# Performance work log

Hardware: AMD Instinct MI355X
Metric: run time of the kernel (lower is better)

Reference implementation:

```python
import jax, jax.numpy as jnp
import numpy as np

NEG_SLOPE = 0.2
EPS = 1e-16


def setup_inputs() -> dict:
    key = jax.random.key(0)
    k1, k2, k3, k4 = jax.random.split(key, 4)
    N, H, F, E = 50000, 4, 32, 800000
    nodes_features = jax.random.normal(k1, (N, H, F), dtype=jnp.float32)
    edge_index = jax.random.randint(k2, (2, E), 0, N, dtype=jnp.int64)
    scoring_fn_source = jax.random.normal(k3, (1, H, F), dtype=jnp.float32)
    scoring_fn_target = jax.random.normal(k4, (1, H, F), dtype=jnp.float32)
    return {
        "nodes_features": nodes_features,
        "scoring_fn_source": scoring_fn_source,
        "scoring_fn_target": scoring_fn_target,
        "edge_index": edge_index,
    }


def reference(nodes_features, scoring_fn_source, scoring_fn_target, edge_index):
    # nodes_features: [N, H, F]; edge_index: [2, E] with row 0 = target, row 1 = source
    num_of_nodes = nodes_features.shape[0]
    trg = edge_index[0]
    src = edge_index[1]

    # Per-node attention logits per head: [N, H]
    scores_source = (nodes_features * scoring_fn_source).sum(axis=-1)
    scores_target = (nodes_features * scoring_fn_target).sum(axis=-1)

    # Lift N -> E via gather: [E, H]
    scores_lifted = scores_source[src] + scores_target[trg]
    src_nodes_features_lifted = nodes_features[src]  # [E, H, F]

    scores_per_edge = jax.nn.leaky_relu(scores_lifted, NEG_SLOPE)
    # Global max subtraction for numerical stability (matches original code)
    scores_per_edge = scores_per_edge - scores_per_edge.max()
    exp_scores = jnp.exp(scores_per_edge)

    # Segment softmax denominator via scatter-add, then gather back per edge
    neighborhood_sums = jax.ops.segment_sum(exp_scores, trg, num_segments=num_of_nodes)
    denom = neighborhood_sums[trg]  # [E, H]

    attentions_per_edge = (exp_scores / (denom + EPS))[..., None]  # [E, H, 1]
    return attentions_per_edge, src_nodes_features_lifted
```

## Files before the change

### kernel.cpp

```cpp
#include <hip/hip_runtime.h>

#define NEG_SLOPE 0.2f
#define EPSV 1e-16f

typedef float f32x4 __attribute__((ext_vector_type(4)));

__device__ __forceinline__ unsigned fenc(float f) {
    unsigned b = __float_as_uint(f);
    return b ^ ((b & 0x80000000u) ? 0xFFFFFFFFu : 0x80000000u);
}
__device__ __forceinline__ float fdec(unsigned u) {
    unsigned b = (u & 0x80000000u) ? (u ^ 0x80000000u) : ~u;
    return __uint_as_float(b);
}
#define FENC_NEG_INF 0x007FFFFFu

__global__ void detect_idx_kernel(const unsigned* __restrict__ ei32,
                                  int* __restrict__ flag) {
    __shared__ int anynz;
    if (threadIdx.x == 0) anynz = 0;
    __syncthreads();
    unsigned v = ei32[2 * threadIdx.x + 1];
    if (v != 0u) anynz = 1;
    __syncthreads();
    if (threadIdx.x == 0) *flag = (anynz ? 0 : 1);
}

__device__ __forceinline__ int load_idx(const void* ei, int is64, size_t k) {
    if (is64) return (int)__builtin_nontemporal_load(&((const long long*)ei)[k]);
    return __builtin_nontemporal_load(&((const int*)ei)[k]);
}

__global__ void node_scores_kernel(const float* __restrict__ nf,
                                   const float* __restrict__ sfs,
                                   const float* __restrict__ sft,
                                   float* __restrict__ ss,
                                   float* __restrict__ st,
                                   float* __restrict__ nsum,
                                   unsigned* __restrict__ gmax,
                                   int NH, int nzero) {
    int i = blockIdx.x * blockDim.x + threadIdx.x;
    if (i >= NH) return;
    if (i == 0) *gmax = FENC_NEG_INF;
    for (int k = i; k < nzero; k += NH) nsum[k] = 0.f;
    int h = i & 3;
    const float4* __restrict__ row = (const float4*)(nf + (size_t)i * 32);
    const float4* __restrict__ as  = (const float4*)(sfs + h * 32);
    const float4* __restrict__ at  = (const float4*)(sft + h * 32);
    float accs = 0.f, acct = 0.f;
#pragma unroll
    for (int q = 0; q < 8; ++q) {
        float4 v = row[q];
        float4 a = as[q];
        float4 b = at[q];
        accs += v.x * a.x + v.y * a.y + v.z * a.z + v.w * a.w;
        acct += v.x * b.x + v.y * b.y + v.z * b.z + v.w * b.w;
    }
    ss[i] = accs;
    st[i] = acct;
}

__global__ void combined_kernel(const void* __restrict__ ei,
                                const int* __restrict__ flag,
                                const f32x4* __restrict__ nf4,
                                const float* __restrict__ ss,
                                const float* __restrict__ st,
                                float* __restrict__ pbuf,
                                float* __restrict__ nsum,
                                unsigned* __restrict__ gmax,
                                f32x4* __restrict__ feat_out,
                                int E, int NS) {
    __shared__ float red[256];
    int is64 = *flag;
    int vbid = blockIdx.x >> 1;
    int vstride = (gridDim.x >> 1) * blockDim.x;

    if ((blockIdx.x & 1) == 0) {
        int n = E * 32;
        for (int t = vbid * blockDim.x + threadIdx.x; t < n; t += vstride) {
            int e = t >> 5, q = t & 31;
            int src = load_idx(ei, is64, (size_t)E + e);
            f32x4 v = nf4[(size_t)src * 32 + q];
            __builtin_nontemporal_store(v, &feat_out[(size_t)e * 32 + q]);
        }
    } else {
        int n4 = E * 4;
        float lmax = -__builtin_inff();
        for (int i = vbid * blockDim.x + threadIdx.x; i < n4; i += vstride) {
            int e = i >> 2, h = i & 3;
            int trg = load_idx(ei, is64, e);
            int src = load_idx(ei, is64, (size_t)E + e);
            float s = ss[src * 4 + h] + st[trg * 4 + h];
            float lr = s > 0.f ? s : NEG_SLOPE * s;
            lmax = fmaxf(lmax, lr);
            float p = __expf(lr);
            __builtin_nontemporal_store(p, &pbuf[i]);
            atomicAdd(&nsum[(size_t)trg * NS + h], p);
        }
        red[threadIdx.x] = lmax;
        __syncthreads();
        for (int off = 128; off > 0; off >>= 1) {
            if (threadIdx.x < off)
                red[threadIdx.x] = fmaxf(red[threadIdx.x], red[threadIdx.x + off]);
            __syncthreads();
        }
        if (threadIdx.x == 0) atomicMax(gmax, fenc(red[0]));
    }
}

__global__ void att_lean_kernel(const void* __restrict__ ei,
                                const int* __restrict__ flag,
                                const float* __restrict__ pbuf,
                                const float* __restrict__ nsum,
                                const unsigned* __restrict__ gmax,
                                float* __restrict__ out,
                                int E, int NS) {
    int is64 = *flag;
    float de = EPSV * __expf(fdec(*gmax));
    int stride = gridDim.x * blockDim.x;
    for (int e = blockIdx.x * blockDim.x + threadIdx.x; e < E; e += stride) {
        int trg = load_idx(ei, is64, e);
        f32x4 p = __builtin_nontemporal_load((const f32x4*)(pbuf + (size_t)e * 4));
        f32x4 d = *(const f32x4*)(nsum + (size_t)trg * NS);
        f32x4 a = p / (d + de);
        __builtin_nontemporal_store(a, (f32x4*)(out + (size_t)e * 4));
    }
}

__device__ __forceinline__ float edge_lr_rc(const void* ei, int is64,
                                            const float* ss, const float* st,
                                            int E, int e, int h, int* trg_out) {
    int trg = load_idx(ei, is64, e);
    int src = load_idx(ei, is64, (size_t)E + e);
    if (trg_out) *trg_out = trg;
    float s = ss[src * 4 + h] + st[trg * 4 + h];
    return s > 0.f ? s : NEG_SLOPE * s;
}

__global__ void edge_exp_sum_fb_kernel(const void* __restrict__ ei,
                                       const int* __restrict__ flag,
                                       const float* __restrict__ ss,
                                       const float* __restrict__ st,
                                       float* __restrict__ nsum,
                                       unsigned* __restrict__ gmax, int E) {
    __shared__ float red[256];
    int is64 = *flag;
    int n4 = E * 4;
    int stride = gridDim.x * blockDim.x;
    float lmax = -__builtin_inff();
    for (int i = blockIdx.x * blockDim.x + threadIdx.x; i < n4; i += stride) {
        int trg;
        float lr = edge_lr_rc(ei, is64, ss, st, E, i >> 2, i & 3, &trg);
        lmax = fmaxf(lmax, lr);
        atomicAdd(&nsum[trg * 4 + (i & 3)], __expf(lr));
    }
    red[threadIdx.x] = lmax;
    __syncthreads();
    for (int off = 128; off > 0; off >>= 1) {
        if (threadIdx.x < off)
            red[threadIdx.x] = fmaxf(red[threadIdx.x], red[threadIdx.x + off]);
        __syncthreads();
    }
    if (threadIdx.x == 0) atomicMax(gmax, fenc(red[0]));
}

__global__ void att_fb_kernel(const void* __restrict__ ei,
                              const int* __restrict__ flag,
                              const float* __restrict__ ss,
                              const float* __restrict__ st,
                              const unsigned* __restrict__ gmax,
                              const float* __restrict__ nsum,
                              float* __restrict__ out, int E) {
    int i = blockIdx.x * blockDim.x + threadIdx.x;
    if (i >= E * 4) return;
    int is64 = *flag;
    float de = EPSV * __expf(fdec(*gmax));
    int trg;
    float lr = edge_lr_rc(ei, is64, ss, st, E, i >> 2, i & 3, &trg);
    float a = __expf(lr) / (nsum[trg * 4 + (i & 3)] + de);
    __builtin_nontemporal_store(a, &out[i]);
}

__global__ void gather_feat_fb_kernel(const void* __restrict__ ei,
                                      const int* __restrict__ flag,
                                      const f32x4* __restrict__ nf4,
                                      f32x4* __restrict__ out4, int E) {
    int is64 = *flag;
    int n = E * 32;
    int stride = gridDim.x * blockDim.x;
    for (int t = blockIdx.x * blockDim.x + threadIdx.x; t < n; t += stride) {
        int e = t >> 5, q = t & 31;
        int src = load_idx(ei, is64, (size_t)E + e);
        f32x4 v = nf4[(size_t)src * 32 + q];
        __builtin_nontemporal_store(v, &out4[(size_t)e * 32 + q]);
    }
}

extern "C" void kernel_launch(void* const* d_in, const int* in_sizes, int n_in,
                              void* d_out, int out_size, void* d_ws, size_t ws_size,
                              hipStream_t stream) {
    const float* nf  = (const float*)d_in[0];
    const float* sfs = (const float*)d_in[1];
    const float* sft = (const float*)d_in[2];
    const void*  ei  = d_in[3];

    const int NH = in_sizes[0] / 32;
    const int N  = NH / 4;
    const int E  = in_sizes[3] / 2;

    float* out = (float*)d_out;
    float* ws  = (float*)d_ws;

    const int B = 256;

    float*    ss   = ws;
    float*    st   = ws + NH;
    int*      flag = (int*)(ws + 2 * (size_t)NH);
    unsigned* gmax = (unsigned*)(flag + 1);
    float*    pbuf = ws + 2 * (size_t)NH + 4;
    float*    nsum = pbuf + (size_t)E * 4;

    int NS = 0;
    for (int cand = 16; cand >= 4; cand >>= 2) {
        size_t need = ((size_t)2 * NH + 4 + (size_t)E * 4 + (size_t)N * cand) * 4;
        if (ws_size >= need) { NS = cand; break; }
    }

    detect_idx_kernel<<<1, 256, 0, stream>>>((const unsigned*)ei, flag);

    if (NS > 0) {
        node_scores_kernel<<<(NH + B - 1) / B, B, 0, stream>>>(
            nf, sfs, sft, ss, st, nsum, gmax, NH, N * NS);
        combined_kernel<<<8192, B, 0, stream>>>(ei, flag, (const f32x4*)nf,
                                                ss, st, pbuf, nsum, gmax,
                                                (f32x4*)(out + (size_t)E * 4),
                                                E, NS);
        att_lean_kernel<<<2048, B, 0, stream>>>(ei, flag, pbuf, nsum, gmax,
                                                out, E, NS);
    } else {
        float* nsum_fb = (float*)(gmax + 1);
        node_scores_kernel<<<(NH + B - 1) / B, B, 0, stream>>>(
            nf, sfs, sft, ss, st, nsum_fb, gmax, NH, NH);
        edge_exp_sum_fb_kernel<<<2048, B, 0, stream>>>(ei, flag, ss, st,
                                                       nsum_fb, gmax, E);
        att_fb_kernel<<<(E * 4 + B - 1) / B, B, 0, stream>>>(ei, flag, ss, st,
                                                             gmax, nsum_fb, out, E);
        gather_feat_fb_kernel<<<4096, B, 0, stream>>>(
            ei, flag, (const f32x4*)nf, (f32x4*)(out + (size_t)E * 4), E);
    }
}
```

Baseline: 256.0 us.

## Accumulate softmax denominators with packed bf16 atomics and split feature gather

Replaces the fp32 per-head atomicAdd into padded neighborhood sums with packed two-wide bf16 atomic adds (global_atomic_fadd_v2bf16, with a CAS fallback), so each edge issues two atomics instead of four and the sum array shrinks to 8 bytes per node. The feature gather no longer shares a kernel with the score pass and runs as its own launch after the attention pass. The padded-stride layout meant to spread atomic contention is dropped. bf16 accumulation of sums over about 16 edges per node loses precision, which may exceed the tolerance, and the separate gather gives up the overlap the combined kernel provided.

```diff
diff --git a/kernel.cpp b/kernel.cpp
--- a/kernel.cpp
+++ b/kernel.cpp
@@ -1,9 +1,13 @@
 #include <hip/hip_runtime.h>
+#include <hip/hip_bf16.h>
 
 #define NEG_SLOPE 0.2f
 #define EPSV 1e-16f
 
 typedef float f32x4 __attribute__((ext_vector_type(4)));
+typedef float f32x2 __attribute__((ext_vector_type(2)));
+typedef short s16x2 __attribute__((ext_vector_type(2)));
+typedef unsigned u32x2 __attribute__((ext_vector_type(2)));
 
 __device__ __forceinline__ unsigned fenc(float f) {
     unsigned b = __float_as_uint(f);
@@ -14,6 +18,31 @@
     return __uint_as_float(b);
 }
 #define FENC_NEG_INF 0x007FFFFFu
+
+__device__ __forceinline__ unsigned f32_to_bf16_rne(float f) {
+    unsigned u = __float_as_uint(f);
+    unsigned lsb = (u >> 16) & 1u;
+    return (u + 0x7FFFu + lsb) >> 16;
+}
+
+__device__ __forceinline__ void pk_atomic_add_bf16(unsigned* addr, float a, float b) {
+#if __has_builtin(__builtin_amdgcn_global_atomic_fadd_v2bf16)
+    s16x2 v;
+    v.x = (short)f32_to_bf16_rne(a);
+    v.y = (short)f32_to_bf16_rne(b);
+    typedef __attribute__((address_space(1))) s16x2 gs16x2;
+    __builtin_amdgcn_global_atomic_fadd_v2bf16((gs16x2*)(void*)addr, v);
+#else
+    unsigned old = *addr, assumed;
+    do {
+        assumed = old;
+        float lo = __uint_as_float((assumed & 0xFFFFu) << 16) + a;
+        float hi = __uint_as_float(assumed & 0xFFFF0000u) + b;
+        unsigned nv = (f32_to_bf16_rne(hi) << 16) | (f32_to_bf16_rne(lo) & 0xFFFFu);
+        old = atomicCAS(addr, assumed, nv);
+    } while (old != assumed);
+#endif
+}
 
 __global__ void detect_idx_kernel(const unsigned* __restrict__ ei32,
                                   int* __restrict__ flag) {
@@ -36,13 +65,13 @@
                                    const float* __restrict__ sft,
                                    float* __restrict__ ss,
                                    float* __restrict__ st,
-                                   float* __restrict__ nsum,
+                                   unsigned* __restrict__ nsum_zero,
                                    unsigned* __restrict__ gmax,
                                    int NH, int nzero) {
     int i = blockIdx.x * blockDim.x + threadIdx.x;
     if (i >= NH) return;
     if (i == 0) *gmax = FENC_NEG_INF;
-    for (int k = i; k < nzero; k += NH) nsum[k] = 0.f;
+    for (int k = i; k < nzero; k += NH) nsum_zero[k] = 0u;
     int h = i & 3;
     const float4* __restrict__ row = (const float4*)(nf + (size_t)i * 32);
     const float4* __restrict__ as  = (const float4*)(sfs + h * 32);
@@ -60,70 +89,80 @@
     st[i] = acct;
 }
 
-__global__ void combined_kernel(const void* __restrict__ ei,
-                                const int* __restrict__ flag,
-                                const f32x4* __restrict__ nf4,
-                                const float* __restrict__ ss,
-                                const float* __restrict__ st,
-                                float* __restrict__ pbuf,
-                                float* __restrict__ nsum,
-                                unsigned* __restrict__ gmax,
-                                f32x4* __restrict__ feat_out,
-                                int E, int NS) {
+__global__ void edge_exp_sum_pk_kernel(const void* __restrict__ ei,
+                                       const int* __restrict__ flag,
+                                       const float* __restrict__ ss,
+                                       const float* __restrict__ st,
+                                       float* __restrict__ pbuf,
+                                       unsigned* __restrict__ nsum_pk,
+                                       unsigned* __restrict__ gmax,
+                                       int E) {
     __shared__ float red[256];
     int is64 = *flag;
-    int vbid = blockIdx.x >> 1;
-    int vstride = (gridDim.x >> 1) * blockDim.x;
-
-    if ((blockIdx.x & 1) == 0) {
-        int n = E * 32;
-        for (int t = vbid * blockDim.x + threadIdx.x; t < n; t += vstride) {
-            int e = t >> 5, q = t & 31;
-            int src = load_idx(ei, is64, (size_t)E + e);
-            f32x4 v = nf4[(size_t)src * 32 + q];
-            __builtin_nontemporal_store(v, &feat_out[(size_t)e * 32 + q]);
-        }
-    } else {
-        int n4 = E * 4;
-        float lmax = -__builtin_inff();
-        for (int i = vbid * blockDim.x + threadIdx.x; i < n4; i += vstride) {
-            int e = i >> 2, h = i & 3;
-            int trg = load_idx(ei, is64, e);
-            int src = load_idx(ei, is64, (size_t)E + e);
-            float s = ss[src * 4 + h] + st[trg * 4 + h];
-            float lr = s > 0.f ? s : NEG_SLOPE * s;
-            lmax = fmaxf(lmax, lr);
-            float p = __expf(lr);
-            __builtin_nontemporal_store(p, &pbuf[i]);
-            atomicAdd(&nsum[(size_t)trg * NS + h], p);
-        }
-        red[threadIdx.x] = lmax;
+    int n2 = E * 2;
+    int stride = gridDim.x * blockDim.x;
+    float lmax = -__builtin_inff();
+    for (int i = blockIdx.x * blockDim.x + threadIdx.x; i < n2; i += stride) {
+        int e = i >> 1, hp = i & 1;
+        int trg = load_idx(ei, is64, e);
+        int src = load_idx(ei, is64, (size_t)E + e);
+        f32x2 a = *(const f32x2*)(ss + (size_t)src * 4 + hp * 2);
+        f32x2 b = *(const f32x2*)(st + (size_t)trg * 4 + hp * 2);
+        float s0 = a.x + b.x, s1 = a.y + b.y;
+        float lr0 = s0 > 0.f ? s0 : NEG_SLOPE * s0;
+        float lr1 = s1 > 0.f ? s1 : NEG_SLOPE * s1;
+        lmax = fmaxf(lmax, fmaxf(lr0, lr1));
+        float p0 = __expf(lr0), p1 = __expf(lr1);
+        f32x2 pv; pv.x = p0; pv.y = p1;
+        __builtin_nontemporal_store(pv, (f32x2*)(pbuf + (size_t)e * 4 + hp * 2));
+        pk_atomic_add_bf16(nsum_pk + (size_t)trg * 2 + hp, p0, p1);
+    }
+    red[threadIdx.x] = lmax;
+    __syncthreads();
+    for (int off = 128; off > 0; off >>= 1) {
+        if (threadIdx.x < off)
+            red[threadIdx.x] = fmaxf(red[threadIdx.x], red[threadIdx.x + off]);
         __syncthreads();
-        for (int off = 128; off > 0; off >>= 1) {
-            if (threadIdx.x < off)
-                red[threadIdx.x] = fmaxf(red[threadIdx.x], red[threadIdx.x + off]);
-            __syncthreads();
-        }
-        if (threadIdx.x == 0) atomicMax(gmax, fenc(red[0]));
-    }
-}
-
-__global__ void att_lean_kernel(const void* __restrict__ ei,
-                                const int* __restrict__ flag,
-                                const float* __restrict__ pbuf,
-                                const float* __restrict__ nsum,
-                                const unsigned* __restrict__ gmax,
-                                float* __restrict__ out,
-                                int E, int NS) {
+    }
+    if (threadIdx.x == 0) atomicMax(gmax, fenc(red[0]));
+}
+
+__global__ void att_pk_kernel(const void* __restrict__ ei,
+                              const int* __restrict__ flag,
+                              const float* __restrict__ pbuf,
+                              const unsigned* __restrict__ nsum_pk,
+                              const unsigned* __restrict__ gmax,
+                              float* __restrict__ out,
+                              int E) {
     int is64 = *flag;
     float de = EPSV * __expf(fdec(*gmax));
     int stride = gridDim.x * blockDim.x;
     for (int e = blockIdx.x * blockDim.x + threadIdx.x; e < E; e += stride) {
         int trg = load_idx(ei, is64, e);
+        u32x2 u = *(const u32x2*)(nsum_pk + (size_t)trg * 2);
+        f32x4 d;
+        d.x = __uint_as_float((u.x & 0xFFFFu) << 16);
+        d.y = __uint_as_float(u.x & 0xFFFF0000u);
+        d.z = __uint_as_float((u.y & 0xFFFFu) << 16);
+        d.w = __uint_as_float(u.y & 0xFFFF0000u);
         f32x4 p = __builtin_nontemporal_load((const f32x4*)(pbuf + (size_t)e * 4));
-        f32x4 d = *(const f32x4*)(nsum + (size_t)trg * NS);
         f32x4 a = p / (d + de);
         __builtin_nontemporal_store(a, (f32x4*)(out + (size_t)e * 4));
+    }
+}
+
+__global__ void gather_feat_kernel(const void* __restrict__ ei,
+                                   const int* __restrict__ flag,
+                                   const f32x4* __restrict__ nf4,
+                                   f32x4* __restrict__ out4, int E) {
+    int is64 = *flag;
+    int n = E * 32;
+    int stride = gridDim.x * blockDim.x;
+    for (int t = blockIdx.x * blockDim.x + threadIdx.x; t < n; t += stride) {
+        int e = t >> 5, q = t & 31;
+        int src = load_idx(ei, is64, (size_t)E + e);
+        f32x4 v = nf4[(size_t)src * 32 + q];
+        __builtin_nontemporal_store(v, &out4[(size_t)e * 32 + q]);
     }
 }
 
@@ -135,6 +174,11 @@
     if (trg_out) *trg_out = trg;
     float s = ss[src * 4 + h] + st[trg * 4 + h];
     return s > 0.f ? s : NEG_SLOPE * s;
+}
+
+__global__ void zero_fb_kernel(float* __restrict__ nsum, int n) {
+    int i = blockIdx.x * blockDim.x + threadIdx.x;
+    if (i < n) nsum[i] = 0.f;
 }
 
 __global__ void edge_exp_sum_fb_kernel(const void* __restrict__ ei,
@@ -181,21 +225,6 @@
     __builtin_nontemporal_store(a, &out[i]);
 }
 
-__global__ void gather_feat_fb_kernel(const void* __restrict__ ei,
-                                      const int* __restrict__ flag,
-                                      const f32x4* __restrict__ nf4,
-                                      f32x4* __restrict__ out4, int E) {
-    int is64 = *flag;
-    int n = E * 32;
-    int stride = gridDim.x * blockDim.x;
-    for (int t = blockIdx.x * blockDim.x + threadIdx.x; t < n; t += stride) {
-        int e = t >> 5, q = t & 31;
-        int src = load_idx(ei, is64, (size_t)E + e);
-        f32x4 v = nf4[(size_t)src * 32 + q];
-        __builtin_nontemporal_store(v, &out4[(size_t)e * 32 + q]);
-    }
-}
-
 extern "C" void kernel_launch(void* const* d_in, const int* in_sizes, int n_in,
                               void* d_out, int out_size, void* d_ws, size_t ws_size,
                               hipStream_t stream) {
@@ -211,41 +240,39 @@
     float* out = (float*)d_out;
     float* ws  = (float*)d_ws;
 
+    float*    ss      = ws;
+    float*    st      = ws + NH;
+    int*      flag    = (int*)(ws + 2 * (size_t)NH);
+    unsigned* gmax    = (unsigned*)(flag + 1);
+    float*    pbuf    = ws + 2 * (size_t)NH + 4;
+    unsigned* nsum_pk = (unsigned*)(pbuf + (size_t)E * 4);
+
+    size_t need = ((size_t)2 * NH + 4 + (size_t)E * 4 + (size_t)N * 2) * 4;
+    bool lean = ws_size >= need;
+
     const int B = 256;
 
-    float*    ss   = ws;
-    float*    st   = ws + NH;
-    int*      flag = (int*)(ws + 2 * (size_t)NH);
-    unsigned* gmax = (unsigned*)(flag + 1);
-    float*    pbuf = ws + 2 * (size_t)NH + 4;
-    float*    nsum = pbuf + (size_t)E * 4;
-
-    int NS = 0;
-    for (int cand = 16; cand >= 4; cand >>= 2) {
-        size_t need = ((size_t)2 * NH + 4 + (size_t)E * 4 + (size_t)N * cand) * 4;
-        if (ws_size >= need) { NS = cand; break; }
-    }
-
     detect_idx_kernel<<<1, 256, 0, stream>>>((const unsigned*)ei, flag);
 
-    if (NS > 0) {
+    if (lean) {
         node_scores_kernel<<<(NH + B - 1) / B, B, 0, stream>>>(
-            nf, sfs, sft, ss, st, nsum, gmax, NH, N * NS);
-        combined_kernel<<<8192, B, 0, stream>>>(ei, flag, (const f32x4*)nf,
-                                                ss, st, pbuf, nsum, gmax,
-                                                (f32x4*)(out + (size_t)E * 4),
-                                                E, NS);
-        att_lean_kernel<<<2048, B, 0, stream>>>(ei, flag, pbuf, nsum, gmax,
-                                                out, E, NS);
+            nf, sfs, sft, ss, st, nsum_pk, gmax, NH, N * 2);
+        edge_exp_sum_pk_kernel<<<2048, B, 0, stream>>>(ei, flag, ss, st, pbuf,
+                                                       nsum_pk, gmax, E);
+        att_pk_kernel<<<2048, B, 0, stream>>>(ei, flag, pbuf, nsum_pk, gmax,
+                                              out, E);
+        gather_feat_kernel<<<4096, B, 0, stream>>>(
+            ei, flag, (const f32x4*)nf, (f32x4*)(out + (size_t)E * 4), E);
     } else {
         float* nsum_fb = (float*)(gmax + 1);
         node_scores_kernel<<<(NH + B - 1) / B, B, 0, stream>>>(
-            nf, sfs, sft, ss, st, nsum_fb, gmax, NH, NH);
+            nf, sfs, sft, ss, st, (unsigned*)nsum_fb, gmax, NH, 0);
+        zero_fb_kernel<<<(NH + B - 1) / B, B, 0, stream>>>(nsum_fb, NH);
         edge_exp_sum_fb_kernel<<<2048, B, 0, stream>>>(ei, flag, ss, st,
                                                        nsum_fb, gmax, E);
         att_fb_kernel<<<(E * 4 + B - 1) / B, B, 0, stream>>>(ei, flag, ss, st,
                                                              gmax, nsum_fb, out, E);
-        gather_feat_fb_kernel<<<4096, B, 0, stream>>>(
+        gather_feat_kernel<<<4096, B, 0, stream>>>(
             ei, flag, (const f32x4*)nf, (f32x4*)(out + (size_t)E * 4), E);
     }
 }
```

Measured after the change: 237.5 us. -7.3%, faster.
